# Optimization experiments

Measured on AMD Instinct MI355X. Metric: run time of the kernel, lower is better.

## Reference

```python
import jax, jax.numpy as jnp
import numpy as np

B, T, N, F = 4, 24, 4096, 32
L = 3  # n_layers

@jax.custom_vjp
def spike_fn(x):
    return (x > 0).astype(x.dtype)

def _spike_fwd(x):
    return spike_fn(x), x

def _spike_bwd(x, g):
    # snntorch ATan surrogate, alpha=2.0: grad = 1 / (1 + (pi*x)^2)
    return (g / (1.0 + (jnp.pi * x) ** 2),)

spike_fn.defvjp(_spike_fwd, _spike_bwd)

def synaptic_step(inp, syn, mem, alpha, beta, thr):
    a = jnp.clip(alpha, 0.0, 1.0)
    b = jnp.clip(beta, 0.0, 1.0)
    reset = jax.lax.stop_gradient(spike_fn(mem - thr))  # spike from previous mem, detached
    syn_new = a * syn + inp
    mem_new = b * mem + syn_new - reset * thr  # subtract reset mechanism
    spk = spike_fn(mem_new - thr)
    return spk, syn_new, mem_new

def _forward(x, alphas, betas, thrs, chain_W, chain_b, lin_out_W, lin_out_b,
             mlp_W1, mlp_b1, prelu_a, mlp_W2, mlp_b2):
    b, t, n, f = x.shape
    x_t = jnp.transpose(x, (1, 0, 2, 3))  # (t, b, n, f)
    syn0 = jnp.zeros((L + 1, b, n, f), x.dtype)
    mem0 = jnp.zeros((L + 1, b, n, f), x.dtype)

    def step(carry, xt):
        syns, mems = carry
        h = xt
        new_syns, new_mems = [], []
        for i in range(L):
            spk, sy, mm = synaptic_step(h, syns[i], mems[i], alphas[i], betas[i], thrs[i])
            new_syns.append(sy); new_mems.append(mm)
            h = spk @ chain_W[i].T + chain_b[i]
        spk, sy, mm = synaptic_step(h, syns[L], mems[L], alphas[L], betas[L], thrs[L])
        new_syns.append(sy); new_mems.append(mm)
        transformed = spk @ lin_out_W.T + lin_out_b  # output_type='spike'
        h1 = transformed @ mlp_W1.T + mlp_b1
        h1 = jnp.where(h1 > 0, h1, prelu_a * h1)
        out_t = h1 @ mlp_W2.T + mlp_b2
        return (jnp.stack(new_syns), jnp.stack(new_mems)), out_t

    _, outs = jax.lax.scan(step, (syn0, mem0), x_t)
    return jnp.transpose(outs, (1, 0, 2, 3))  # (b, t, n, f)

def setup_inputs() -> dict:
    key = jax.random.key(0)
    ks = jax.random.split(key, 10)
    f = F
    s = 1.0 / np.sqrt(f)
    inp = {
        'x': jax.random.normal(ks[0], (B, T, N, F), jnp.float32),
        'alphas': jnp.full((L + 1,), 0.9, jnp.float32),
        'betas': jnp.full((L + 1,), 0.8, jnp.float32),
        'thrs': jnp.ones((L + 1,), jnp.float32),
        'chain_W': jax.random.uniform(ks[1], (L, f, f), jnp.float32, -s, s),
        'chain_b': jax.random.uniform(ks[2], (L, f), jnp.float32, -s, s),
        'lin_out_W': jax.random.uniform(ks[3], (f, f), jnp.float32, -s, s),
        'lin_out_b': jax.random.uniform(ks[4], (f,), jnp.float32, -s, s),
        'mlp_W1': jax.random.uniform(ks[5], (2 * f, f), jnp.float32, -s, s),
        'mlp_b1': jax.random.uniform(ks[6], (2 * f,), jnp.float32, -s, s),
        'prelu_a': jnp.asarray(0.25, jnp.float32),
        'mlp_W2': jax.random.uniform(ks[7], (f, 2 * f), jnp.float32, -1.0 / np.sqrt(2 * f), 1.0 / np.sqrt(2 * f)),
        'mlp_b2': jax.random.uniform(ks[8], (f,), jnp.float32, -1.0 / np.sqrt(2 * f), 1.0 / np.sqrt(2 * f)),
    }
    return inp

def reference(x, alphas, betas, thrs, chain_W, chain_b, lin_out_W, lin_out_b,
              mlp_W1, mlp_b1, prelu_a, mlp_W2, mlp_b2):
    return _forward(x, alphas, betas, thrs, chain_W, chain_b, lin_out_W, lin_out_b,
                    mlp_W1, mlp_b1, prelu_a, mlp_W2, mlp_b2)
```

## Files before the change

kernel.cpp:

```cpp
#include <hip/hip_runtime.h>
#include <hip/hip_bf16.h>


namespace {
constexpr int kB = 4;
constexpr int kT = 24;
constexpr int kN = 4096;
constexpr int kF = 32;
constexpr int kNF = kN * kF;

typedef __attribute__((ext_vector_type(8))) short short8v;
typedef __attribute__((ext_vector_type(4))) float float4v;

__device__ __forceinline__ short bfc(float f) {
    return (short)__bfloat16_as_ushort(__float2bfloat16(f));
}
__device__ __forceinline__ float bfc_back(short s) {
    return __bfloat162float(__ushort_as_bfloat16((unsigned short)s));
}
__device__ __forceinline__ float uni(float v) {
    return __int_as_float(__builtin_amdgcn_readfirstlane(__float_as_int(v)));
}

__device__ __forceinline__ void cvt_hilo(const float* v, short8v& hi, short8v& lo) {
#pragma unroll
    for (int e = 0; e < 8; ++e) {
        const short h = bfc(v[e]);
        hi[e] = h;
        lo[e] = bfc(v[e] - bfc_back(h));
    }
}

__global__ __launch_bounds__(512, 2)
void snn_fused(const float* __restrict__ x,
               const float* __restrict__ alphas,
               const float* __restrict__ betas,
               const float* __restrict__ thrs,
               const float* __restrict__ chain_W,
               const float* __restrict__ chain_b,
               const float* __restrict__ lin_W,
               const float* __restrict__ lin_b,
               const float* __restrict__ W1,
               const float* __restrict__ b1,
               const float* __restrict__ prelu_a,
               const float* __restrict__ W2,
               const float* __restrict__ b2,
               float* __restrict__ out)
{
    const int tid  = threadIdx.x;
    const int lane = tid & 63;
    const int wid  = tid >> 6;
    const int r    = lane >> 3;
    const int q    = lane & 7;
    const int l16  = lane & 15;
    const int lg   = lane >> 4;

    const int base = (blockIdx.x * 8 + wid) * 8;
    const int row  = base + r;
    const int b    = row >> 12;
    const int n    = row & (kN - 1);
    const int bq   = base >> 12;
    const int n0   = base & (kN - 1);

    __shared__ float    lutQ[3][8][16][8][4];
    __shared__ float    gbuf[8][16][68];
    __shared__ short8v  wfrag[12][64];
    __shared__ unsigned mlds[8][2][8];

#pragma unroll
    for (int c = 0; c < 2; ++c) {
        const int idx = tid + c * 512;
        if (idx < 768) {
            const int mat = idx >> 8;
            const int g   = (idx >> 5) & 7;
            const int jj  = idx & 31;
            const float* wsrc = chain_W + ((mat * kF + jj) * kF + g * 4);
            const float4 w = *reinterpret_cast<const float4*>(wsrc);
            const float bias = (g == 0) ? chain_b[mat * kF + jj] : 0.0f;
            float s[16];
            s[0]  = 0.0f;
            s[1]  = w.x;         s[2]  = w.y;         s[3]  = w.x + w.y;
            s[4]  = w.z;         s[5]  = w.x + w.z;   s[6]  = w.y + w.z;
            s[7]  = s[3] + w.z;  s[8]  = w.w;         s[9]  = w.x + w.w;
            s[10] = w.y + w.w;   s[11] = s[3] + w.w;  s[12] = w.z + w.w;
            s[13] = s[5] + w.w;  s[14] = s[6] + w.w;  s[15] = s[7] + w.w;
#pragma unroll
            for (int nb = 0; nb < 16; ++nb)
                lutQ[mat][g][nb][jj & 7][jj >> 3] = s[nb] + bias;
        }
    }

#pragma unroll
    for (int c = 0; c < 2; ++c) {
        const int idx = tid + c * 512;
        if (idx < 768) {
            const int f     = idx >> 6;
            const int lane2 = idx & 63;
            const int l16b  = lane2 & 15, lgb = lane2 >> 4;
            short8v fr;
            if (f < 4) {
                const int cc = f >> 1, sp = f & 1;
#pragma unroll
                for (int e = 0; e < 8; ++e) {
                    const float w  = lin_W[(cc * 16 + l16b) * 32 + lgb * 8 + e];
                    const short s0 = bfc(w);
                    fr[e] = sp ? bfc(w - bfc_back(s0)) : s0;
                }
            } else if (f < 8) {
                const int c0 = f - 4;
#pragma unroll
                for (int e = 0; e < 8; ++e)
                    fr[e] = bfc(W1[(c0 * 16 + l16b) * 32 + lgb * 8 + e]);
            } else {
                const int c2 = (f - 8) >> 1, kb = (f - 8) & 1;
#pragma unroll
                for (int e = 0; e < 8; ++e)
                    fr[e] = bfc(W2[(c2 * 16 + l16b) * 64 + kb * 32 + lgb * 8 + e]);
            }
            wfrag[f][lane2] = fr;
        }
    }
    __syncthreads();

    float al[4], be[4], th[4];
#pragma unroll
    for (int i = 0; i < 4; ++i) {
        al[i] = uni(fminf(fmaxf(alphas[i], 0.0f), 1.0f));
        be[i] = uni(fminf(fmaxf(betas[i],  0.0f), 1.0f));
        th[i] = uni(thrs[i]);
    }
    const float pa = uni(prelu_a[0]);

    float lbv[2], b1v[4], b2v[2];
#pragma unroll
    for (int c = 0; c < 2; ++c)  lbv[c]  = lin_b[c * 16 + l16];
#pragma unroll
    for (int c0 = 0; c0 < 4; ++c0) b1v[c0] = b1[c0 * 16 + l16];
#pragma unroll
    for (int c2 = 0; c2 < 2; ++c2) b2v[c2] = b2[c2 * 16 + l16];

    float syn[4][4], mem[4][4];
#pragma unroll
    for (int i = 0; i < 4; ++i)
#pragma unroll
        for (int s = 0; s < 4; ++s) { syn[i][s] = 0.0f; mem[i][s] = 0.0f; }

    const float* xp = x + (size_t)(b * kT * kN + n) * kF + q;

    float xv[4];
#pragma unroll
    for (int s = 0; s < 4; ++s) xv[s] = xp[8 * s];

    for (int tb = 0; tb < 12; ++tb) {
        for (int tt = 0; tt < 2; ++tt) {
            const int t = tb * 2 + tt;
            float xn[4] = {0.f, 0.f, 0.f, 0.f};
            if (t + 1 < kT) {
#pragma unroll
                for (int s = 0; s < 4; ++s) xn[s] = xp[(size_t)(t + 1) * kNF + 8 * s];
            }

            float hh[4];
#pragma unroll
            for (int s = 0; s < 4; ++s) hh[s] = xv[s];

#pragma unroll
            for (int i = 0; i < 4; ++i) {
                bool sp[4];
#pragma unroll
                for (int s = 0; s < 4; ++s) {
                    const float rst = ((mem[i][s] - th[i]) > 0.0f) ? 1.0f : 0.0f;
                    syn[i][s] = al[i] * syn[i][s] + hh[s];
                    mem[i][s] = be[i] * mem[i][s] + syn[i][s] - rst * th[i];
                    sp[s] = (mem[i][s] - th[i]) > 0.0f;
                }
                unsigned long long bal0 = __ballot(sp[0]);
                unsigned long long bal1 = __ballot(sp[1]);
                unsigned long long bal2 = __ballot(sp[2]);
                unsigned long long bal3 = __ballot(sp[3]);
                const unsigned f0 = (unsigned)((bal0 >> (r * 8)) & 0xFFull);
                const unsigned f1 = (unsigned)((bal1 >> (r * 8)) & 0xFFull);
                const unsigned f2 = (unsigned)((bal2 >> (r * 8)) & 0xFFull);
                const unsigned f3 = (unsigned)((bal3 >> (r * 8)) & 0xFFull);
                const unsigned m32 = f0 | (f1 << 8) | (f2 << 16) | (f3 << 24);

                if (i < 3) {
                    float4v vv[8];
#pragma unroll
                    for (int g = 0; g < 8; ++g) {
                        const unsigned nib = (m32 >> (4 * g)) & 15u;
                        vv[g] = *reinterpret_cast<const float4v*>(&lutQ[i][g][nib][q][0]);
                    }
#pragma unroll
                    for (int s = 0; s < 4; ++s)
                        hh[s] = ((vv[0][s] + vv[1][s]) + (vv[2][s] + vv[3][s]))
                              + ((vv[4][s] + vv[5][s]) + (vv[6][s] + vv[7][s]));
                } else if (q == 0) {
                    mlds[wid][tt][r] = m32;
                }
            }

#pragma unroll
            for (int s = 0; s < 4; ++s) xv[s] = xn[s];
        }

        const unsigned m = mlds[wid][l16 >> 3][l16 & 7];
        short8v aspk;
#pragma unroll
        for (int e = 0; e < 8; ++e)
            aspk[e] = ((m >> (lg * 8 + e)) & 1u) ? (short)0x3F80 : (short)0;

        const short8v lf00 = wfrag[0][lane];
        const short8v lf01 = wfrag[1][lane];
        const short8v lf10 = wfrag[2][lane];
        const short8v lf11 = wfrag[3][lane];

        float4v t0 = {lbv[0], lbv[0], lbv[0], lbv[0]};
        float4v t1 = {lbv[1], lbv[1], lbv[1], lbv[1]};
        t0 = __builtin_amdgcn_mfma_f32_16x16x32_bf16(aspk, lf00, t0, 0, 0, 0);
        t0 = __builtin_amdgcn_mfma_f32_16x16x32_bf16(aspk, lf01, t0, 0, 0, 0);
        t1 = __builtin_amdgcn_mfma_f32_16x16x32_bf16(aspk, lf10, t1, 0, 0, 0);
        t1 = __builtin_amdgcn_mfma_f32_16x16x32_bf16(aspk, lf11, t1, 0, 0, 0);

#pragma unroll
        for (int rr = 0; rr < 4; ++rr) {
            gbuf[wid][lg * 4 + rr][l16]      = t0[rr];
            gbuf[wid][lg * 4 + rr][16 + l16] = t1[rr];
        }
        float tv[8];
        {
            const float* pt = &gbuf[wid][l16][lg * 8];
            *reinterpret_cast<float4*>(tv)     = *reinterpret_cast<const float4*>(pt);
            *reinterpret_cast<float4*>(tv + 4) = *reinterpret_cast<const float4*>(pt + 4);
        }
        short8v ahi, alo;
        cvt_hilo(tv, ahi, alo);

        float4v acc[4];
#pragma unroll
        for (int c0 = 0; c0 < 4; ++c0) {
            const short8v wf = wfrag[4 + c0][lane];
            float4v c = {b1v[c0], b1v[c0], b1v[c0], b1v[c0]};
            c = __builtin_amdgcn_mfma_f32_16x16x32_bf16(ahi, wf, c, 0, 0, 0);
            c = __builtin_amdgcn_mfma_f32_16x16x32_bf16(alo, wf, c, 0, 0, 0);
            acc[c0] = c;
        }

#pragma unroll
        for (int c0 = 0; c0 < 4; ++c0) {
#pragma unroll
            for (int rr = 0; rr < 4; ++rr) {
                float v = acc[c0][rr];
                v = (v > 0.0f) ? v : pa * v;
                gbuf[wid][lg * 4 + rr][c0 * 16 + l16] = v;
            }
        }

        float4v o[2];
#pragma unroll
        for (int c2 = 0; c2 < 2; ++c2)
            o[c2] = float4v{b2v[c2], b2v[c2], b2v[c2], b2v[c2]};
#pragma unroll
        for (int kb = 0; kb < 2; ++kb) {
            float gv[8];
            const float* pg = &gbuf[wid][l16][kb * 32 + lg * 8];
            *reinterpret_cast<float4*>(gv)     = *reinterpret_cast<const float4*>(pg);
            *reinterpret_cast<float4*>(gv + 4) = *reinterpret_cast<const float4*>(pg + 4);
            short8v ghi, glo;
            cvt_hilo(gv, ghi, glo);
#pragma unroll
            for (int c2 = 0; c2 < 2; ++c2) {
                const short8v wf = wfrag[8 + c2 * 2 + kb][lane];
                o[c2] = __builtin_amdgcn_mfma_f32_16x16x32_bf16(ghi, wf, o[c2], 0, 0, 0);
                o[c2] = __builtin_amdgcn_mfma_f32_16x16x32_bf16(glo, wf, o[c2], 0, 0, 0);
            }
        }

#pragma unroll
        for (int c2 = 0; c2 < 2; ++c2) {
#pragma unroll
            for (int rr = 0; rr < 4; ++rr) {
                const int v = lg * 4 + rr;
                const size_t orow =
                    ((size_t)(bq * kT + tb * 2 + (v >> 3)) * kN + (n0 + (v & 7))) * kF;
                out[orow + c2 * 16 + l16] = o[c2][rr];
            }
        }
    }
}
}

extern "C" void kernel_launch(void* const* d_in, const int* in_sizes, int n_in,
                              void* d_out, int out_size, void* d_ws, size_t ws_size,
                              hipStream_t stream) {
    const float* x        = (const float*)d_in[0];
    const float* alphas   = (const float*)d_in[1];
    const float* betas    = (const float*)d_in[2];
    const float* thrs     = (const float*)d_in[3];
    const float* chain_W  = (const float*)d_in[4];
    const float* chain_b  = (const float*)d_in[5];
    const float* lin_W    = (const float*)d_in[6];
    const float* lin_b    = (const float*)d_in[7];
    const float* W1       = (const float*)d_in[8];
    const float* b1       = (const float*)d_in[9];
    const float* prelu_a  = (const float*)d_in[10];
    const float* W2       = (const float*)d_in[11];
    const float* b2       = (const float*)d_in[12];
    float* out            = (float*)d_out;

    hipLaunchKernelGGL(snn_fused, dim3(256), dim3(512), 0, stream,
                       x, alphas, betas, thrs, chain_W, chain_b, lin_W, lin_b,
                       W1, b1, prelu_a, W2, b2, out);
}
```

Baseline: 50.17 us.

## Chain MLP MFMAs in registers via transposed operands and permuted K mapping

After: 47.28 us. -5.8%, faster.

```diff
diff --git a/kernel.cpp b/kernel.cpp
--- a/kernel.cpp
+++ b/kernel.cpp
@@ -21,14 +21,8 @@
 __device__ __forceinline__ float uni(float v) {
     return __int_as_float(__builtin_amdgcn_readfirstlane(__float_as_int(v)));
 }
-
-__device__ __forceinline__ void cvt_hilo(const float* v, short8v& hi, short8v& lo) {
-#pragma unroll
-    for (int e = 0; e < 8; ++e) {
-        const short h = bfc(v[e]);
-        hi[e] = h;
-        lo[e] = bfc(v[e] - bfc_back(h));
-    }
+__device__ __forceinline__ constexpr int kmap(int lg, int e) {
+    return (e < 4) ? (lg * 4 + e) : (16 + lg * 4 + (e - 4));
 }
 
 __global__ __launch_bounds__(512, 2)
@@ -63,7 +57,6 @@
     const int n0   = base & (kN - 1);
 
     __shared__ float    lutQ[3][8][16][8][4];
-    __shared__ float    gbuf[8][16][68];
     __shared__ short8v  wfrag[12][64];
     __shared__ unsigned mlds[8][2][8];
 
@@ -102,7 +95,7 @@
                 const int cc = f >> 1, sp = f & 1;
 #pragma unroll
                 for (int e = 0; e < 8; ++e) {
-                    const float w  = lin_W[(cc * 16 + l16b) * 32 + lgb * 8 + e];
+                    const float w  = lin_W[(cc * 16 + l16b) * 32 + kmap(lgb, e)];
                     const short s0 = bfc(w);
                     fr[e] = sp ? bfc(w - bfc_back(s0)) : s0;
                 }
@@ -110,12 +103,12 @@
                 const int c0 = f - 4;
 #pragma unroll
                 for (int e = 0; e < 8; ++e)
-                    fr[e] = bfc(W1[(c0 * 16 + l16b) * 32 + lgb * 8 + e]);
+                    fr[e] = bfc(W1[(c0 * 16 + l16b) * 32 + kmap(lgb, e)]);
             } else {
                 const int c2 = (f - 8) >> 1, kb = (f - 8) & 1;
 #pragma unroll
                 for (int e = 0; e < 8; ++e)
-                    fr[e] = bfc(W2[(c2 * 16 + l16b) * 64 + kb * 32 + lgb * 8 + e]);
+                    fr[e] = bfc(W2[(c2 * 16 + l16b) * 64 + kb * 32 + kmap(lgb, e)]);
             }
             wfrag[f][lane2] = fr;
         }
@@ -130,14 +123,6 @@
         th[i] = uni(thrs[i]);
     }
     const float pa = uni(prelu_a[0]);
-
-    float lbv[2], b1v[4], b2v[2];
-#pragma unroll
-    for (int c = 0; c < 2; ++c)  lbv[c]  = lin_b[c * 16 + l16];
-#pragma unroll
-    for (int c0 = 0; c0 < 4; ++c0) b1v[c0] = b1[c0 * 16 + l16];
-#pragma unroll
-    for (int c2 = 0; c2 < 2; ++c2) b2v[c2] = b2[c2 * 16 + l16];
 
     float syn[4][4], mem[4][4];
 #pragma unroll
@@ -208,83 +193,64 @@
         short8v aspk;
 #pragma unroll
         for (int e = 0; e < 8; ++e)
-            aspk[e] = ((m >> (lg * 8 + e)) & 1u) ? (short)0x3F80 : (short)0;
-
-        const short8v lf00 = wfrag[0][lane];
-        const short8v lf01 = wfrag[1][lane];
-        const short8v lf10 = wfrag[2][lane];
-        const short8v lf11 = wfrag[3][lane];
-
-        float4v t0 = {lbv[0], lbv[0], lbv[0], lbv[0]};
-        float4v t1 = {lbv[1], lbv[1], lbv[1], lbv[1]};
-        t0 = __builtin_amdgcn_mfma_f32_16x16x32_bf16(aspk, lf00, t0, 0, 0, 0);
-        t0 = __builtin_amdgcn_mfma_f32_16x16x32_bf16(aspk, lf01, t0, 0, 0, 0);
-        t1 = __builtin_amdgcn_mfma_f32_16x16x32_bf16(aspk, lf10, t1, 0, 0, 0);
-        t1 = __builtin_amdgcn_mfma_f32_16x16x32_bf16(aspk, lf11, t1, 0, 0, 0);
-
-#pragma unroll
-        for (int rr = 0; rr < 4; ++rr) {
-            gbuf[wid][lg * 4 + rr][l16]      = t0[rr];
-            gbuf[wid][lg * 4 + rr][16 + l16] = t1[rr];
-        }
-        float tv[8];
-        {
-            const float* pt = &gbuf[wid][l16][lg * 8];
-            *reinterpret_cast<float4*>(tv)     = *reinterpret_cast<const float4*>(pt);
-            *reinterpret_cast<float4*>(tv + 4) = *reinterpret_cast<const float4*>(pt + 4);
-        }
-        short8v ahi, alo;
-        cvt_hilo(tv, ahi, alo);
-
-        float4v acc[4];
-#pragma unroll
-        for (int c0 = 0; c0 < 4; ++c0) {
-            const short8v wf = wfrag[4 + c0][lane];
-            float4v c = {b1v[c0], b1v[c0], b1v[c0], b1v[c0]};
-            c = __builtin_amdgcn_mfma_f32_16x16x32_bf16(ahi, wf, c, 0, 0, 0);
-            c = __builtin_amdgcn_mfma_f32_16x16x32_bf16(alo, wf, c, 0, 0, 0);
-            acc[c0] = c;
-        }
-
-#pragma unroll
-        for (int c0 = 0; c0 < 4; ++c0) {
+            aspk[e] = ((m >> kmap(lg, e)) & 1u) ? (short)0x3F80 : (short)0;
+
+        const float4 lb0 = *reinterpret_cast<const float4*>(lin_b + lg * 4);
+        const float4 lb1 = *reinterpret_cast<const float4*>(lin_b + 16 + lg * 4);
+        float4v t0 = {lb0.x, lb0.y, lb0.z, lb0.w};
+        float4v t1 = {lb1.x, lb1.y, lb1.z, lb1.w};
+        t0 = __builtin_amdgcn_mfma_f32_16x16x32_bf16(wfrag[0][lane], aspk, t0, 0, 0, 0);
+        t0 = __builtin_amdgcn_mfma_f32_16x16x32_bf16(wfrag[1][lane], aspk, t0, 0, 0, 0);
+        t1 = __builtin_amdgcn_mfma_f32_16x16x32_bf16(wfrag[2][lane], aspk, t1, 0, 0, 0);
+        t1 = __builtin_amdgcn_mfma_f32_16x16x32_bf16(wfrag[3][lane], aspk, t1, 0, 0, 0);
+
+        short8v thi, tlo;
+#pragma unroll
+        for (int e = 0; e < 4; ++e) {
+            const short h0 = bfc(t0[e]);
+            thi[e] = h0; tlo[e] = bfc(t0[e] - bfc_back(h0));
+            const short h1 = bfc(t1[e]);
+            thi[4 + e] = h1; tlo[4 + e] = bfc(t1[e] - bfc_back(h1));
+        }
+
+        float g[16];
+#pragma unroll
+        for (int q4 = 0; q4 < 4; ++q4) {
+            const float4 b14 = *reinterpret_cast<const float4*>(b1 + q4 * 16 + lg * 4);
+            float4v c = {b14.x, b14.y, b14.z, b14.w};
+            const short8v wf = wfrag[4 + q4][lane];
+            c = __builtin_amdgcn_mfma_f32_16x16x32_bf16(wf, thi, c, 0, 0, 0);
+            c = __builtin_amdgcn_mfma_f32_16x16x32_bf16(wf, tlo, c, 0, 0, 0);
 #pragma unroll
             for (int rr = 0; rr < 4; ++rr) {
-                float v = acc[c0][rr];
-                v = (v > 0.0f) ? v : pa * v;
-                gbuf[wid][lg * 4 + rr][c0 * 16 + l16] = v;
-            }
-        }
-
-        float4v o[2];
-#pragma unroll
-        for (int c2 = 0; c2 < 2; ++c2)
-            o[c2] = float4v{b2v[c2], b2v[c2], b2v[c2], b2v[c2]};
-#pragma unroll
-        for (int kb = 0; kb < 2; ++kb) {
-            float gv[8];
-            const float* pg = &gbuf[wid][l16][kb * 32 + lg * 8];
-            *reinterpret_cast<float4*>(gv)     = *reinterpret_cast<const float4*>(pg);
-            *reinterpret_cast<float4*>(gv + 4) = *reinterpret_cast<const float4*>(pg + 4);
-            short8v ghi, glo;
-            cvt_hilo(gv, ghi, glo);
-#pragma unroll
-            for (int c2 = 0; c2 < 2; ++c2) {
-                const short8v wf = wfrag[8 + c2 * 2 + kb][lane];
-                o[c2] = __builtin_amdgcn_mfma_f32_16x16x32_bf16(ghi, wf, o[c2], 0, 0, 0);
-                o[c2] = __builtin_amdgcn_mfma_f32_16x16x32_bf16(glo, wf, o[c2], 0, 0, 0);
-            }
-        }
-
-#pragma unroll
-        for (int c2 = 0; c2 < 2; ++c2) {
-#pragma unroll
-            for (int rr = 0; rr < 4; ++rr) {
-                const int v = lg * 4 + rr;
-                const size_t orow =
-                    ((size_t)(bq * kT + tb * 2 + (v >> 3)) * kN + (n0 + (v & 7))) * kF;
-                out[orow + c2 * 16 + l16] = o[c2][rr];
-            }
+                const float v = c[rr];
+                g[q4 * 4 + rr] = (v > 0.0f) ? v : pa * v;
+            }
+        }
+
+        short8v gh[2], gl[2];
+#pragma unroll
+        for (int kb = 0; kb < 2; ++kb)
+#pragma unroll
+            for (int e = 0; e < 8; ++e) {
+                const float v = g[kb * 8 + e];
+                const short h0 = bfc(v);
+                gh[kb][e] = h0;
+                gl[kb][e] = bfc(v - bfc_back(h0));
+            }
+
+        const size_t orow =
+            ((size_t)(bq * kT + tb * 2 + (l16 >> 3)) * kN + (n0 + (l16 & 7))) * kF;
+#pragma unroll
+        for (int oq = 0; oq < 2; ++oq) {
+            const float4 b24 = *reinterpret_cast<const float4*>(b2 + oq * 16 + lg * 4);
+            float4v o = {b24.x, b24.y, b24.z, b24.w};
+            o = __builtin_amdgcn_mfma_f32_16x16x32_bf16(wfrag[8 + oq * 2 + 0][lane], gh[0], o, 0, 0, 0);
+            o = __builtin_amdgcn_mfma_f32_16x16x32_bf16(wfrag[8 + oq * 2 + 0][lane], gl[0], o, 0, 0, 0);
+            o = __builtin_amdgcn_mfma_f32_16x16x32_bf16(wfrag[8 + oq * 2 + 1][lane], gh[1], o, 0, 0, 0);
+            o = __builtin_amdgcn_mfma_f32_16x16x32_bf16(wfrag[8 + oq * 2 + 1][lane], gl[1], o, 0, 0, 0);
+            float4 st = {o[0], o[1], o[2], o[3]};
+            *reinterpret_cast<float4*>(out + orow + oq * 16 + lg * 4) = st;
         }
     }
 }
```
